# Kernel tuning notes

Hardware: AMD Instinct MI355X
Metric: run time of the kernel (lower is better)

The kernel has to match this reference:

```python
import jax, jax.numpy as jnp
import numpy as np


def setup_inputs() -> dict:
    key = jax.random.key(0)
    k1, k2, k3, k4 = jax.random.split(key, 4)
    B, Q, K, H, D = 2, 2048, 2048, 16, 128
    qs = jax.random.normal(k1, (B, Q, H, D), dtype=jnp.float32)
    ks = jax.random.normal(k2, (B, K, H, D), dtype=jnp.float32)
    vs = jax.random.normal(k3, (B, K, H, D), dtype=jnp.float32)
    valid_lens = jax.random.randint(k4, (B,), 1, K + 1, dtype=jnp.int32)
    return {"qs": qs, "ks": ks, "vs": vs, "valid_lens": valid_lens}


def reference(qs, ks, vs, valid_lens):
    B, Q, H, D = qs.shape
    K = ks.shape[1]
    # rearrange 'B L H D -> (B H) L D'
    q = qs.transpose(0, 2, 1, 3).reshape(B * H, Q, D)
    k = ks.transpose(0, 2, 1, 3).reshape(B * H, K, D)
    v = vs.transpose(0, 2, 1, 3).reshape(B * H, K, D)
    # DotScorer: scaled dot product -> (B*H, Q, K)
    scores = jnp.einsum('bqd,bkd->bqk', q, k) / jnp.sqrt(jnp.float32(D))
    # mask_attn: key positions >= valid_len get large negative score
    vl = jnp.repeat(valid_lens, H)                         # (B*H,)
    mask = jnp.arange(K)[None, None, :] < vl[:, None, None]
    scores = jnp.where(mask, scores, jnp.float32(-1e6))
    attn = jax.nn.softmax(scores, axis=-1)
    # dropout is identity (p_dropout=0 / not training)
    ctx = attn @ v                                         # (B*H, Q, D)
    ctx = ctx.reshape(B, H, Q, D).transpose(0, 2, 1, 3)    # (B, Q, H, D)
    return ctx, attn.reshape(B, H, Q, K)
```

## Files before the change

### kernel.cpp

```cpp
#include <hip/hip_runtime.h>
#include <hip/hip_bf16.h>
#include <stdint.h>

#define B_ 2
#define Qn 2048
#define Kn 2048
#define Hn 16
#define Dn 128
#define QT 128
#define HD (Hn*Dn)

typedef __bf16 bf16x8 __attribute__((ext_vector_type(8)));
typedef __bf16 bf16x4 __attribute__((ext_vector_type(4)));
typedef float f32x4 __attribute__((ext_vector_type(4)));
typedef float f32x16 __attribute__((ext_vector_type(16)));
typedef unsigned short u16x8 __attribute__((ext_vector_type(8)));

union BF8 { __bf16 e[8]; bf16x8 v; };
union U16x8 { unsigned short u[8]; u16x8 v; };

#define SCALE 0.088388347648318447f
#define SCL2  (0.088388347648318447f * 1.4426950408889634f)

#if __has_builtin(__builtin_amdgcn_exp2f)
#define EXP2(x) __builtin_amdgcn_exp2f(x)
#else
#define EXP2(x) exp2f(x)
#endif

__device__ __forceinline__ bf16x4 cvt4(f32x4 a) {
  bf16x4 r;
  r[0] = (__bf16)a[0]; r[1] = (__bf16)a[1];
  r[2] = (__bf16)a[2]; r[3] = (__bf16)a[3];
  return r;
}

__global__ __launch_bounds__(256) void conv_k(const float* __restrict__ ks,
                                              const int* __restrict__ vlen,
                                              unsigned short* __restrict__ kws) {
  const int blk = blockIdx.x;
  const int bh = blk >> 4, t = blk & 15;
  const int b = bh >> 4, h = bh & 15;
  const int nkt = (vlen[b] + 63) >> 6;
  if (t * 2 >= nkt) return;
  const int tid = threadIdx.x;
  const float* src = ks + ((size_t)(b * Kn + t * 128) * Hn + h) * Dn;
  unsigned short* dst = kws + (size_t)blk * 16384;
  #pragma unroll
  for (int i = 0; i < 8; ++i) {
    int idx = i * 256 + tid;
    int row = idx >> 4, sp = idx & 15;
    int slot = (sp - row) & 15;
    const float* s2 = src + (size_t)row * HD + slot * 8;
    f32x4 a0 = *(const f32x4*)s2;
    f32x4 a1 = *(const f32x4*)(s2 + 4);
    U16x8 o;
    *(bf16x4*)&o.u[0] = cvt4(a0);
    *(bf16x4*)&o.u[4] = cvt4(a1);
    *(u16x8*)(dst + (size_t)idx * 8) = o.v;
  }
}

__global__ __launch_bounds__(256) void conv_v(const float* __restrict__ vs,
                                              const int* __restrict__ vlen,
                                              unsigned short* __restrict__ vws) {
  __shared__ unsigned short l[64 * 132];
  const int blk = blockIdx.x;
  const int bh = blk >> 5, t = blk & 31;
  const int b = bh >> 4, h = bh & 15;
  const int nkt = (vlen[b] + 63) >> 6;
  if (t >= nkt) return;
  const int tid = threadIdx.x;
  const float* src = vs + ((size_t)(b * Kn + t * 64) * Hn + h) * Dn;
  #pragma unroll
  for (int i = 0; i < 8; ++i) {
    int idx = i * 256 + tid;
    int k = idx >> 5, dc = idx & 31;
    f32x4 a = *(const f32x4*)(src + (size_t)k * HD + dc * 4);
    *(bf16x4*)&l[k * 132 + dc * 4] = cvt4(a);
  }
  __syncthreads();
  unsigned short* dst = vws + (size_t)blk * 8192;
  #pragma unroll
  for (int i = 0; i < 4; ++i) {
    int idx = i * 256 + tid;
    int d = idx >> 3, ds = idx & 7;
    int c = (ds - d) & 7;
    int kb = ((c >> 2) * 32) + (((c >> 1) & 1) * 16) + ((c & 1) * 4);
    U16x8 o;
    #pragma unroll
    for (int j = 0; j < 4; ++j) {
      o.u[j]     = l[(kb + j) * 132 + d];
      o.u[4 + j] = l[(kb + 8 + j) * 132 + d];
    }
    *(u16x8*)(dst + (size_t)idx * 8) = o.v;
  }
}

__device__ __forceinline__ void dma16(const void* g, void* l) {
  __builtin_amdgcn_global_load_lds((const __attribute__((address_space(1))) void*)g,
                                   (__attribute__((address_space(3))) void*)l, 16, 0, 0);
}
__device__ __forceinline__ void dma_tile(const char* gsrc, char* lds, int tid, int n4k) {
  const int off  = tid * 16;
  const int woff = (tid & 192) * 16;
  #pragma unroll
  for (int i = 0; i < n4k; ++i)
    dma16(gsrc + i * 4096 + off, lds + i * 4096 + woff);
}

#define WAIT0BAR do { \
  asm volatile("s_waitcnt vmcnt(0)" ::: "memory"); \
  __builtin_amdgcn_s_barrier(); \
  __builtin_amdgcn_sched_barrier(0); } while (0)

#define WAIT16BAR do { \
  asm volatile("s_waitcnt vmcnt(16)" ::: "memory"); \
  __builtin_amdgcn_s_barrier(); \
  __builtin_amdgcn_sched_barrier(0); } while (0)

__global__ __launch_bounds__(256, 2) void attn_fwd(
    const float* __restrict__ qs, const int* __restrict__ vlen,
    const char* __restrict__ kimg, const char* __restrict__ vimg,
    float* __restrict__ ctx_out, float* __restrict__ attn_out)
{
  __shared__ __align__(16) char smraw[65536];

  const int tid = threadIdx.x, wave = tid >> 6, lane = tid & 63;
  const int l31 = lane & 31, hi = lane >> 5;

  const int L   = blockIdx.x;
  const int xcd = L & 7;
  const int i5  = L >> 3;
  const int bh  = ((i5 & 3) << 3) + xcd;
  const int qt  = i5 >> 2;
  const int b   = bh >> 4, h = bh & 15;
  const int vl  = vlen[b];
  const int qbw = qt * QT + wave * 32;

  int vaddrK[8], vaddrV[4];
  #pragma unroll
  for (int s = 0; s < 8; ++s)
    vaddrK[s] = l31 * 256 + (((2 * s + hi + l31) & 15) << 4);
  #pragma unroll
  for (int jj = 0; jj < 4; ++jj)
    vaddrV[jj] = l31 * 128 + ((((hi + 2 * jj) + l31) & 7) << 4);

  BF8 qf[8];
  {
    const float* qrow = qs + (((size_t)(b * Qn + qbw + l31)) * Hn + h) * Dn;
    #pragma unroll
    for (int s = 0; s < 8; ++s) {
      int d0 = s * 16 + hi * 8;
      f32x4 a0 = *(const f32x4*)(qrow + d0);
      f32x4 a1 = *(const f32x4*)(qrow + d0 + 4);
      #pragma unroll
      for (int jj = 0; jj < 4; ++jj) {
        qf[s].e[jj]     = (__bf16)(a0[jj] * SCL2);
        qf[s].e[4 + jj] = (__bf16)(a1[jj] * SCL2);
      }
    }
  }

  const char* kimg_bh = kimg + ((size_t)(bh * 16) << 15);
  const char* vimg_bh = vimg + ((size_t)(bh * 32) << 14);

  const int nkt  = (vl + 63) >> 6;
  const int nkt2 = (vl + 127) >> 7;
  const int col0 = nkt * 64;

  f32x4 rsv = {0.f, 0.f, 0.f, 0.f};
  f32x16 ctxa[4];
  #pragma unroll
  for (int ch = 0; ch < 4; ++ch)
    #pragma unroll
    for (int i = 0; i < 16; ++i) ctxa[ch][i] = 0.f;

  {
    const bool hasb = (vl & 63) != 0;
    dma_tile(kimg_bh, smraw, tid, 4);
    dma_tile(vimg_bh, smraw + 32768, tid, 4);
    WAIT0BAR;
    for (int t = 0; t < nkt; ++t) {
      const int cur = t & 1;
      if (t + 1 < nkt) {
        const int tn = t + 1;
        dma_tile(kimg_bh + ((size_t)(tn >> 1) << 15) + ((size_t)(tn & 1) << 14),
                 smraw + ((cur ^ 1) << 14), tid, 4);
        dma_tile(vimg_bh + ((size_t)tn << 14), smraw + 32768 + ((cur ^ 1) << 14), tid, 4);
      }
      const bool mb = hasb && (t == nkt - 1);
      const char* kb_l = smraw + (cur << 14);
      const char* vb_l = smraw + 32768 + (cur << 14);
      #pragma unroll
      for (int m = 0; m < 2; ++m) {
        f32x16 acc;
        #pragma unroll
        for (int i = 0; i < 16; ++i) acc[i] = 0.f;
        #pragma unroll
        for (int s = 0; s < 8; ++s) {
          BF8 kf; kf.v = *(const bf16x8*)(kb_l + m * 8192 + vaddrK[s]);
          acc = __builtin_amdgcn_mfma_f32_32x32x16_bf16(kf.v, qf[s].v, acc, 0, 0, 0);
        }
        const int kb0 = t * 64 + m * 32;
        BF8 pf0, pf1;
        #pragma unroll
        for (int r4 = 0; r4 < 4; ++r4) {
          #pragma unroll
          for (int rr = 0; rr < 4; ++rr) {
            float e;
            if (!mb) e = EXP2(acc[r4 * 4 + rr]);
            else {
              int key = kb0 + r4 * 8 + hi * 4 + rr;
              e = (key < vl) ? EXP2(acc[r4 * 4 + rr]) : 0.f;
            }
            rsv[rr] += e;
            if (r4 < 2) pf0.e[r4 * 4 + rr] = (__bf16)e;
            else        pf1.e[(r4 - 2) * 4 + rr] = (__bf16)e;
          }
        }
        #pragma unroll
        for (int ch = 0; ch < 4; ++ch) {
          BF8 v0; v0.v = *(const bf16x8*)(vb_l + ch * 4096 + vaddrV[2 * m]);
          ctxa[ch] = __builtin_amdgcn_mfma_f32_32x32x16_bf16(v0.v, pf0.v, ctxa[ch], 0, 0, 0);
          BF8 v1; v1.v = *(const bf16x8*)(vb_l + ch * 4096 + vaddrV[2 * m + 1]);
          ctxa[ch] = __builtin_amdgcn_mfma_f32_32x32x16_bf16(v1.v, pf1.v, ctxa[ch], 0, 0, 0);
        }
      }
      WAIT0BAR;
    }
  }
  float rs = (rsv[0] + rsv[1]) + (rsv[2] + rsv[3]);
  rs += __shfl_xor(rs, 32);
  const float inv = 1.0f / rs;

  {
    const f32x4 z4 = {0.f, 0.f, 0.f, 0.f};
    #pragma unroll 1
    for (int r = 0; r < 32; ++r) {
      float* zp = attn_out + ((size_t)bh * Qn + qbw + r) * Kn;
      for (int c4 = col0 + lane * 4; c4 < Kn; c4 += 256)
        *(f32x4*)(zp + c4) = z4;
    }
  }

  {
    const bool hasb2 = (vl & 127) != 0;
    dma_tile(kimg_bh, smraw, tid, 8);
    WAIT0BAR;
    float* rowp = attn_out + ((size_t)bh * Qn + qbw + l31) * Kn;
    for (int t = 0; t < nkt2; ++t) {
      const int cur = t & 1;
      if (t + 1 < nkt2)
        dma_tile(kimg_bh + ((size_t)(t + 1) << 15), smraw + ((cur ^ 1) << 15), tid, 8);
      const bool mb = hasb2 && (t == nkt2 - 1);
      const char* kb_l = smraw + (cur << 15);
      #pragma unroll
      for (int m = 0; m < 4; ++m) {
        f32x16 acc;
        #pragma unroll
        for (int i = 0; i < 16; ++i) acc[i] = 0.f;
        #pragma unroll
        for (int s = 0; s < 8; ++s) {
          BF8 kf; kf.v = *(const bf16x8*)(kb_l + m * 8192 + vaddrK[s]);
          acc = __builtin_amdgcn_mfma_f32_32x32x16_bf16(kf.v, qf[s].v, acc, 0, 0, 0);
        }
        const int kb0 = t * 128 + m * 32;
        #pragma unroll
        for (int r4 = 0; r4 < 4; ++r4) {
          f32x4 p;
          if (!mb) {
            #pragma unroll
            for (int rr = 0; rr < 4; ++rr) p[rr] = EXP2(acc[r4 * 4 + rr]) * inv;
          } else {
            #pragma unroll
            for (int rr = 0; rr < 4; ++rr) {
              int key = kb0 + r4 * 8 + hi * 4 + rr;
              p[rr] = (key < vl) ? EXP2(acc[r4 * 4 + rr]) * inv : 0.f;
            }
          }
          *(f32x4*)(rowp + kb0 + r4 * 8 + hi * 4) = p;
        }
      }
      WAIT16BAR;
    }
  }

  float* cp = ctx_out + (((size_t)(b * Qn + qbw + l31)) * Hn + h) * Dn;
  #pragma unroll
  for (int ch = 0; ch < 4; ++ch)
    #pragma unroll
    for (int r4 = 0; r4 < 4; ++r4) {
      f32x4 o;
      #pragma unroll
      for (int rr = 0; rr < 4; ++rr) o[rr] = ctxa[ch][r4 * 4 + rr] * inv;
      *(f32x4*)(cp + ch * 32 + r4 * 8 + hi * 4) = o;
    }
}

#define KT 64
#define KT1 128
#define KROW 132
#define VROW 72
struct SMp2f { unsigned short K[2][KT][KROW]; unsigned short V[2][Dn][VROW]; };
union SMuf { SMp2f p2; unsigned short K1[2][KT1][KROW]; };

__device__ __forceinline__ void bar_lgkm() {
  asm volatile("s_waitcnt lgkmcnt(0)" ::: "memory");
  __builtin_amdgcn_s_barrier();
  __builtin_amdgcn_sched_barrier(0);
}
__device__ __forceinline__ void fb_stage_k64(const float* kb, unsigned short (*dst)[KROW], int tid) {
  #pragma unroll
  for (int ii = 0; ii < 8; ++ii) {
    int chunk = ii * 256 + tid;
    int row = chunk >> 5, cv = chunk & 31;
    f32x4 a = *(const f32x4*)(kb + (size_t)row * HD + cv * 4);
    *(bf16x4*)&dst[row][cv * 4] = cvt4(a);
  }
}
__device__ __forceinline__ void fb_stage_k128(const float* kb, unsigned short (*dst)[KROW], int tid) {
  #pragma unroll
  for (int ii = 0; ii < 16; ++ii) {
    int chunk = ii * 256 + tid;
    int row = chunk >> 5, cv = chunk & 31;
    f32x4 a = *(const f32x4*)(kb + (size_t)row * HD + cv * 4);
    *(bf16x4*)&dst[row][cv * 4] = cvt4(a);
  }
}
__device__ __forceinline__ void fb_stage_v64(const float* vb, unsigned short (*dst)[VROW], int tid) {
  int d = tid & 127, t0 = tid >> 7;
  const float* colp = vb + d;
  #pragma unroll
  for (int rr = 0; rr < 4; ++rr) {
    int idx = rr * 2 + t0;
    int base = (idx >> 2) * 32 + ((idx >> 1) & 1) * 16 + (idx & 1) * 4;
    BF8 t;
    #pragma unroll
    for (int jj = 0; jj < 4; ++jj) {
      t.e[jj]     = (__bf16)colp[(size_t)(base + jj) * HD];
      t.e[4 + jj] = (__bf16)colp[(size_t)(base + 8 + jj) * HD];
    }
    *(bf16x8*)&dst[d][idx * 8] = t.v;
  }
}
__global__ __launch_bounds__(256, 2) void attn_fwd_fb(
    const float* __restrict__ qs, const float* __restrict__ ks,
    const float* __restrict__ vs, const int* __restrict__ vlen,
    float* __restrict__ ctx_out, float* __restrict__ attn_out)
{
  __shared__ __align__(16) SMuf sm;
  const int tid = threadIdx.x, wave = tid >> 6, lane = tid & 63;
  const int l31 = lane & 31, hi = lane >> 5;
  const int L = blockIdx.x, xcd = L & 7, i5 = L >> 3;
  const int bh = ((i5 & 3) << 3) + xcd, qt = i5 >> 2;
  const int b = bh >> 4, h = bh & 15;
  const int vl = vlen[b];
  const int qbw = qt * QT + wave * 32;
  BF8 qf[8];
  {
    const float* qrow = qs + (((size_t)(b * Qn + qbw + l31)) * Hn + h) * Dn;
    #pragma unroll
    for (int s = 0; s < 8; ++s) {
      int d0 = s * 16 + hi * 8;
      f32x4 a0 = *(const f32x4*)(qrow + d0);
      f32x4 a1 = *(const f32x4*)(qrow + d0 + 4);
      #pragma unroll
      for (int jj = 0; jj < 4; ++jj) {
        qf[s].e[jj] = (__bf16)(a0[jj] * SCL2);
        qf[s].e[4 + jj] = (__bf16)(a1[jj] * SCL2);
      }
    }
  }
  const float* kbase = ks + ((size_t)b * Kn * Hn + h) * Dn;
  const float* vbase = vs + ((size_t)b * Kn * Hn + h) * Dn;
  f32x4 rsv = {0.f, 0.f, 0.f, 0.f};
  {
    const int nkt1 = (vl + KT1 - 1) / KT1;
    const bool hasb1 = (vl & (KT1 - 1)) != 0;
    fb_stage_k128(kbase, sm.K1[0], tid);
    bar_lgkm();
    for (int t = 0; t < nkt1; ++t) {
      const int cur = t & 1;
      if (t + 1 < nkt1) fb_stage_k128(kbase + (size_t)(t + 1) * KT1 * HD, sm.K1[cur ^ 1], tid);
      const bool mb = hasb1 && (t == nkt1 - 1);
      #pragma unroll
      for (int m = 0; m < 4; ++m) {
        f32x16 acc;
        #pragma unroll
        for (int i = 0; i < 16; ++i) acc[i] = 0.f;
        #pragma unroll
        for (int s = 0; s < 8; ++s) {
          BF8 kf; kf.v = *(const bf16x8*)&sm.K1[cur][m * 32 + l31][s * 16 + hi * 8];
          acc = __builtin_amdgcn_mfma_f32_32x32x16_bf16(kf.v, qf[s].v, acc, 0, 0, 0);
        }
        if (!mb) {
          #pragma unroll
          for (int reg = 0; reg < 16; ++reg) rsv[reg & 3] += EXP2(acc[reg]);
        } else {
          const int kb0 = t * KT1 + m * 32 + hi * 4;
          #pragma unroll
          for (int reg = 0; reg < 16; ++reg) {
            int key = kb0 + (reg & 3) + 8 * (reg >> 2);
            rsv[reg & 3] += (key < vl) ? EXP2(acc[reg]) : 0.f;
          }
        }
      }
      bar_lgkm();
    }
  }
  float rs = (rsv[0] + rsv[1]) + (rsv[2] + rsv[3]);
  rs += __shfl_xor(rs, 32);
  const float inv = 1.0f / rs;
  f32x16 ctxa[4];
  #pragma unroll
  for (int ch = 0; ch < 4; ++ch)
    #pragma unroll
    for (int i = 0; i < 16; ++i) ctxa[ch][i] = 0.f;
  const int nkt = (vl + KT - 1) / KT;
  const bool hasb2 = (vl & (KT - 1)) != 0;
  fb_stage_k64(kbase, sm.p2.K[0], tid);
  fb_stage_v64(vbase, sm.p2.V[0], tid);
  bar_lgkm();
  float* rowp = attn_out + ((size_t)bh * Qn + qbw + l31) * Kn;
  for (int t = 0; t < nkt; ++t) {
    const int cur = t & 1;
    if (t + 1 < nkt) {
      fb_stage_k64(kbase + (size_t)(t + 1) * KT * HD, sm.p2.K[cur ^ 1], tid);
      fb_stage_v64(vbase + (size_t)(t + 1) * KT * HD, sm.p2.V[cur ^ 1], tid);
    }
    const bool mb = hasb2 && (t == nkt - 1);
    #pragma unroll
    for (int m = 0; m < 2; ++m) {
      f32x16 acc;
      #pragma unroll
      for (int i = 0; i < 16; ++i) acc[i] = 0.f;
      #pragma unroll
      for (int s = 0; s < 8; ++s) {
        BF8 kf; kf.v = *(const bf16x8*)&sm.p2.K[cur][m * 32 + l31][s * 16 + hi * 8];
        acc = __builtin_amdgcn_mfma_f32_32x32x16_bf16(kf.v, qf[s].v, acc, 0, 0, 0);
      }
      const int kb0 = t * KT + m * 32;
      BF8 pf0, pf1;
      #pragma unroll
      for (int r4 = 0; r4 < 4; ++r4) {
        f32x4 p;
        if (!mb) {
          #pragma unroll
          for (int rr = 0; rr < 4; ++rr) p[rr] = EXP2(acc[r4 * 4 + rr]) * inv;
        } else {
          #pragma unroll
          for (int rr = 0; rr < 4; ++rr) {
            int key = kb0 + r4 * 8 + hi * 4 + rr;
            p[rr] = (key < vl) ? EXP2(acc[r4 * 4 + rr]) * inv : 0.f;
          }
        }
        #pragma unroll
        for (int rr = 0; rr < 4; ++rr) {
          if (r4 < 2) pf0.e[r4 * 4 + rr] = (__bf16)p[rr];
          else        pf1.e[(r4 - 2) * 4 + rr] = (__bf16)p[rr];
        }
        *(f32x4*)(rowp + kb0 + r4 * 8 + hi * 4) = p;
      }
      #pragma unroll
      for (int ch = 0; ch < 4; ++ch) {
        BF8 v0; v0.v = *(const bf16x8*)&sm.p2.V[cur][ch * 32 + l31][(m * 4 + hi) * 8];
        ctxa[ch] = __builtin_amdgcn_mfma_f32_32x32x16_bf16(v0.v, pf0.v, ctxa[ch], 0, 0, 0);
        BF8 v1; v1.v = *(const bf16x8*)&sm.p2.V[cur][ch * 32 + l31][(m * 4 + 2 + hi) * 8];
        ctxa[ch] = __builtin_amdgcn_mfma_f32_32x32x16_bf16(v1.v, pf1.v, ctxa[ch], 0, 0, 0);
      }
    }
    bar_lgkm();
  }
  const int col0 = nkt * KT;
  #pragma unroll 1
  for (int r = 0; r < 32; ++r) {
    float* zp = attn_out + ((size_t)bh * Qn + qbw + r) * Kn;
    for (int c4 = col0 + lane * 4; c4 < Kn; c4 += 256)
      *(f32x4*)(zp + c4) = (f32x4){0.f, 0.f, 0.f, 0.f};
  }
  float* cp = ctx_out + (((size_t)(b * Qn + qbw + l31)) * Hn + h) * Dn;
  #pragma unroll
  for (int ch = 0; ch < 4; ++ch)
    #pragma unroll
    for (int r4 = 0; r4 < 4; ++r4) {
      f32x4 o;
      #pragma unroll
      for (int rr = 0; rr < 4; ++rr) o[rr] = ctxa[ch][r4 * 4 + rr];
      *(f32x4*)(cp + ch * 32 + r4 * 8 + hi * 4) = o;
    }
}

extern "C" void kernel_launch(void* const* d_in, const int* in_sizes, int n_in,
                              void* d_out, int out_size, void* d_ws, size_t ws_size,
                              hipStream_t stream) {
  const float* qs   = (const float*)d_in[0];
  const float* ks   = (const float*)d_in[1];
  const float* vs   = (const float*)d_in[2];
  const int*   vlen = (const int*)d_in[3];
  float* ctx  = (float*)d_out;
  float* attn = ctx + (size_t)B_ * Qn * Hn * Dn;

  if (ws_size >= ((size_t)32 << 20)) {
    unsigned short* kws = (unsigned short*)d_ws;
    unsigned short* vws = kws + ((size_t)8 << 20);
    conv_k<<<dim3(512), 256, 0, stream>>>(ks, vlen, kws);
    conv_v<<<dim3(1024), 256, 0, stream>>>(vs, vlen, vws);
    attn_fwd<<<dim3((Qn / QT) * B_ * Hn), 256, 0, stream>>>(
        qs, vlen, (const char*)kws, (const char*)vws, ctx, attn);
  } else {
    attn_fwd_fb<<<dim3((Qn / QT) * B_ * Hn), 256, 0, stream>>>(qs, ks, vs, vlen, ctx, attn);
  }
}
```

Baseline: 186.9 us.

## Merge K/V conversion kernels and interleave attn zero-fill with first pass

Merges the K and V bf16 conversion kernels into one launch that dispatches on block index, saving a kernel launch and the gap between the two. Moves the zero-filling of masked attention columns out of a separate serial loop and into the first-pass tile loop, issuing 8 zero stores per iteration. The barrier is relaxed to vmcnt(8) so those stores can stay in flight behind the compute, and leftover stores run after the loop. This adds clamped index arithmetic that may rewrite the same addresses more than once, and it depends on the vmcnt accounting being right with respect to the DMA loads.

```diff
diff --git a/kernel.cpp b/kernel.cpp
--- a/kernel.cpp
+++ b/kernel.cpp
@@ -35,65 +35,64 @@
   return r;
 }
 
-__global__ __launch_bounds__(256) void conv_k(const float* __restrict__ ks,
-                                              const int* __restrict__ vlen,
-                                              unsigned short* __restrict__ kws) {
-  const int blk = blockIdx.x;
-  const int bh = blk >> 4, t = blk & 15;
-  const int b = bh >> 4, h = bh & 15;
-  const int nkt = (vlen[b] + 63) >> 6;
-  if (t * 2 >= nkt) return;
+__global__ __launch_bounds__(256) void conv_kv(const float* __restrict__ ks,
+                                               const float* __restrict__ vs,
+                                               const int* __restrict__ vlen,
+                                               unsigned short* __restrict__ kws,
+                                               unsigned short* __restrict__ vws) {
+  __shared__ unsigned short l[64 * 132];
   const int tid = threadIdx.x;
-  const float* src = ks + ((size_t)(b * Kn + t * 128) * Hn + h) * Dn;
-  unsigned short* dst = kws + (size_t)blk * 16384;
-  #pragma unroll
-  for (int i = 0; i < 8; ++i) {
-    int idx = i * 256 + tid;
-    int row = idx >> 4, sp = idx & 15;
-    int slot = (sp - row) & 15;
-    const float* s2 = src + (size_t)row * HD + slot * 8;
-    f32x4 a0 = *(const f32x4*)s2;
-    f32x4 a1 = *(const f32x4*)(s2 + 4);
-    U16x8 o;
-    *(bf16x4*)&o.u[0] = cvt4(a0);
-    *(bf16x4*)&o.u[4] = cvt4(a1);
-    *(u16x8*)(dst + (size_t)idx * 8) = o.v;
-  }
-}
-
-__global__ __launch_bounds__(256) void conv_v(const float* __restrict__ vs,
-                                              const int* __restrict__ vlen,
-                                              unsigned short* __restrict__ vws) {
-  __shared__ unsigned short l[64 * 132];
-  const int blk = blockIdx.x;
-  const int bh = blk >> 5, t = blk & 31;
-  const int b = bh >> 4, h = bh & 15;
-  const int nkt = (vlen[b] + 63) >> 6;
-  if (t >= nkt) return;
-  const int tid = threadIdx.x;
-  const float* src = vs + ((size_t)(b * Kn + t * 64) * Hn + h) * Dn;
-  #pragma unroll
-  for (int i = 0; i < 8; ++i) {
-    int idx = i * 256 + tid;
-    int k = idx >> 5, dc = idx & 31;
-    f32x4 a = *(const f32x4*)(src + (size_t)k * HD + dc * 4);
-    *(bf16x4*)&l[k * 132 + dc * 4] = cvt4(a);
-  }
-  __syncthreads();
-  unsigned short* dst = vws + (size_t)blk * 8192;
-  #pragma unroll
-  for (int i = 0; i < 4; ++i) {
-    int idx = i * 256 + tid;
-    int d = idx >> 3, ds = idx & 7;
-    int c = (ds - d) & 7;
-    int kb = ((c >> 2) * 32) + (((c >> 1) & 1) * 16) + ((c & 1) * 4);
-    U16x8 o;
-    #pragma unroll
-    for (int j = 0; j < 4; ++j) {
-      o.u[j]     = l[(kb + j) * 132 + d];
-      o.u[4 + j] = l[(kb + 8 + j) * 132 + d];
-    }
-    *(u16x8*)(dst + (size_t)idx * 8) = o.v;
+  if (blockIdx.x < 512) {
+    const int blk = blockIdx.x;
+    const int bh = blk >> 4, t = blk & 15;
+    const int b = bh >> 4, h = bh & 15;
+    const int nkt = (vlen[b] + 63) >> 6;
+    if (t * 2 >= nkt) return;
+    const float* src = ks + ((size_t)(b * Kn + t * 128) * Hn + h) * Dn;
+    unsigned short* dst = kws + (size_t)blk * 16384;
+    #pragma unroll
+    for (int i = 0; i < 8; ++i) {
+      int idx = i * 256 + tid;
+      int row = idx >> 4, sp = idx & 15;
+      int slot = (sp - row) & 15;
+      const float* s2 = src + (size_t)row * HD + slot * 8;
+      f32x4 a0 = *(const f32x4*)s2;
+      f32x4 a1 = *(const f32x4*)(s2 + 4);
+      U16x8 o;
+      *(bf16x4*)&o.u[0] = cvt4(a0);
+      *(bf16x4*)&o.u[4] = cvt4(a1);
+      *(u16x8*)(dst + (size_t)idx * 8) = o.v;
+    }
+  } else {
+    const int blk = blockIdx.x - 512;
+    const int bh = blk >> 5, t = blk & 31;
+    const int b = bh >> 4, h = bh & 15;
+    const int nkt = (vlen[b] + 63) >> 6;
+    if (t >= nkt) return;
+    const float* src = vs + ((size_t)(b * Kn + t * 64) * Hn + h) * Dn;
+    #pragma unroll
+    for (int i = 0; i < 8; ++i) {
+      int idx = i * 256 + tid;
+      int k = idx >> 5, dc = idx & 31;
+      f32x4 a = *(const f32x4*)(src + (size_t)k * HD + dc * 4);
+      *(bf16x4*)&l[k * 132 + dc * 4] = cvt4(a);
+    }
+    __syncthreads();
+    unsigned short* dst = vws + (size_t)blk * 8192;
+    #pragma unroll
+    for (int i = 0; i < 4; ++i) {
+      int idx = i * 256 + tid;
+      int d = idx >> 3, ds = idx & 7;
+      int c = (ds - d) & 7;
+      int kb = ((c >> 2) * 32) + (((c >> 1) & 1) * 16) + ((c & 1) * 4);
+      U16x8 o;
+      #pragma unroll
+      for (int j = 0; j < 4; ++j) {
+        o.u[j]     = l[(kb + j) * 132 + d];
+        o.u[4 + j] = l[(kb + 8 + j) * 132 + d];
+      }
+      *(u16x8*)(dst + (size_t)idx * 8) = o.v;
+    }
   }
 }
 
@@ -111,6 +110,11 @@
 
 #define WAIT0BAR do { \
   asm volatile("s_waitcnt vmcnt(0)" ::: "memory"); \
+  __builtin_amdgcn_s_barrier(); \
+  __builtin_amdgcn_sched_barrier(0); } while (0)
+
+#define WAIT8BAR do { \
+  asm volatile("s_waitcnt vmcnt(8)" ::: "memory"); \
   __builtin_amdgcn_s_barrier(); \
   __builtin_amdgcn_sched_barrier(0); } while (0)
 
@@ -168,6 +172,19 @@
   const int nkt  = (vl + 63) >> 6;
   const int nkt2 = (vl + 127) >> 7;
   const int col0 = nkt * 64;
+  const int col0_4  = col0 >> 2;
+  const int zrounds = (512 - col0_4 + 63) >> 6;
+  const f32x4 z4 = {0.f, 0.f, 0.f, 0.f};
+  const bool has_zero = (col0 < Kn);
+
+  #define ZSTORE(idx) do { \
+    int row_ = qbw + ((idx) & 31); \
+    int rnd_ = (idx) >> 5; \
+    rnd_ = (rnd_ > zrounds - 1) ? (zrounds - 1) : rnd_; \
+    int c4_ = col0_4 + rnd_ * 64 + lane; \
+    c4_ = (c4_ > 511) ? 511 : c4_; \
+    *(f32x4*)(attn_out + ((size_t)bh * Qn + row_) * Kn + (size_t)c4_ * 4) = z4; \
+  } while (0)
 
   f32x4 rsv = {0.f, 0.f, 0.f, 0.f};
   f32x16 ctxa[4];
@@ -227,21 +244,22 @@
           ctxa[ch] = __builtin_amdgcn_mfma_f32_32x32x16_bf16(v1.v, pf1.v, ctxa[ch], 0, 0, 0);
         }
       }
-      WAIT0BAR;
+      if (has_zero) {
+        const int zb = t * 8;
+        #pragma unroll
+        for (int zi = 0; zi < 8; ++zi) ZSTORE(zb + zi);
+        WAIT8BAR;
+      } else {
+        WAIT0BAR;
+      }
     }
   }
   float rs = (rsv[0] + rsv[1]) + (rsv[2] + rsv[3]);
   rs += __shfl_xor(rs, 32);
   const float inv = 1.0f / rs;
 
-  {
-    const f32x4 z4 = {0.f, 0.f, 0.f, 0.f};
-    #pragma unroll 1
-    for (int r = 0; r < 32; ++r) {
-      float* zp = attn_out + ((size_t)bh * Qn + qbw + r) * Kn;
-      for (int c4 = col0 + lane * 4; c4 < Kn; c4 += 256)
-        *(f32x4*)(zp + c4) = z4;
-    }
+  if (has_zero) {
+    for (int idx = nkt * 8; idx < 32 * zrounds; ++idx) ZSTORE(idx);
   }
 
   {
@@ -296,6 +314,7 @@
       for (int rr = 0; rr < 4; ++rr) o[rr] = ctxa[ch][r4 * 4 + rr] * inv;
       *(f32x4*)(cp + ch * 32 + r4 * 8 + hi * 4) = o;
     }
+  #undef ZSTORE
 }
 
 #define KT 64
@@ -504,8 +523,7 @@
   if (ws_size >= ((size_t)32 << 20)) {
     unsigned short* kws = (unsigned short*)d_ws;
     unsigned short* vws = kws + ((size_t)8 << 20);
-    conv_k<<<dim3(512), 256, 0, stream>>>(ks, vlen, kws);
-    conv_v<<<dim3(1024), 256, 0, stream>>>(vs, vlen, vws);
+    conv_kv<<<dim3(1536), 256, 0, stream>>>(ks, vs, vlen, kws, vws);
     attn_fwd<<<dim3((Qn / QT) * B_ * Hn), 256, 0, stream>>>(
         qs, vlen, (const char*)kws, (const char*)vws, ctx, attn);
   } else {
```

New measurement: 199.3 us. 6.7% more time.
